# Kernel optimization log

Hardware: AMD Instinct MI355X
Metric: run time of the kernel (lower is better)

The kernel has to match this reference:

```python
import jax, jax.numpy as jnp
import numpy as np

B, IN, H = 8192, 1024, 2048

def setup_inputs() -> dict:
    key = jax.random.key(0)
    k1, k2, k3, k4, k5 = jax.random.split(key, 5)
    prev_state = jax.random.normal(k1, (B, H), dtype=jnp.float32)
    x = jax.random.normal(k2, (B, IN), dtype=jnp.float32)
    input_weights = jax.random.normal(k3, (H, IN), dtype=jnp.float32) / IN ** 0.5
    input_bias = jnp.zeros((H,), dtype=jnp.float32)
    recurrent_weights = jax.random.normal(k4, (H, H), dtype=jnp.float32) / H ** 0.5
    U_z = jax.random.normal(k5, (H, H), dtype=jnp.float32) / H ** 0.5
    b_u = jnp.zeros((H,), dtype=jnp.float32)
    return {"prev_state": prev_state, "input": x,
            "input_weights": input_weights, "input_bias": input_bias,
            "recurrent_weights": recurrent_weights, "U_z": U_z, "b_u": b_u}

def reference(prev_state, input, input_weights, input_bias, recurrent_weights, U_z, b_u):
    # z = tanh(x @ W_x^T + b_x)
    z = jnp.tanh(input @ input_weights.T + input_bias)
    # u = sigmoid(h @ W_h^T + z @ U_z^T + b_u)
    u = jax.nn.sigmoid(prev_state @ recurrent_weights.T + z @ U_z.T + b_u)
    # convex combination of previous state and candidate
    state = u * prev_state + (1.0 - u) * z
    return state
```

## Files before the change

kernel.cpp:

```cpp
#include <hip/hip_runtime.h>
#include <hip/hip_bf16.h>
#include <cstdint>
#include <cstddef>

#define DEVFN static __device__ __forceinline__

typedef __attribute__((ext_vector_type(8))) short bf16x8;
typedef __attribute__((ext_vector_type(4))) float f32x4;

static constexpr int kB = 8192;
static constexpr int kIN = 1024;
static constexpr int kH = 2048;

DEVFN unsigned short f32_to_bf16(float f) {
  union { float f; unsigned int u; } v; v.f = f;
  unsigned int x = v.u;
  x += 0x7fffu + ((x >> 16) & 1u);
  return (unsigned short)(x >> 16);
}
DEVFN float bf16_to_f32(unsigned short u) {
  union { unsigned int u; float f; } v; v.u = (unsigned int)u << 16;
  return v.f;
}

__global__ void cast_strided(const float* __restrict__ src, unsigned short* __restrict__ dst,
                             int n, int srcWshift, int dstStride, int dstOff) {
  int i = (blockIdx.x * blockDim.x + threadIdx.x) * 4;
  if (i >= n) return;
  float4 v = *(const float4*)(src + i);
  int row = i >> srcWshift;
  int col = i - (row << srcWshift);
  unsigned short* d = dst + (size_t)row * dstStride + dstOff + col;
  ushort4 o;
  o.x = f32_to_bf16(v.x); o.y = f32_to_bf16(v.y);
  o.z = f32_to_bf16(v.z); o.w = f32_to_bf16(v.w);
  *(ushort4*)d = o;
}

typedef const __attribute__((address_space(1))) unsigned int* gptr_t;
typedef __attribute__((address_space(3))) unsigned int* lptr_t;
DEVFN void gload16(const unsigned short* g, unsigned short* l) {
  __builtin_amdgcn_global_load_lds((gptr_t)g, (lptr_t)l, 16, 0, 0);
}

DEVFN void barpin() {
  __builtin_amdgcn_s_barrier();
  __builtin_amdgcn_sched_barrier(0);
}
#define LGKM0() asm volatile("s_waitcnt lgkmcnt(0)" ::: "memory")
#define VMC4()  asm volatile("s_waitcnt vmcnt(4)" ::: "memory")


template<int BUF, int QM>
DEVFN void ldA(bf16x8 (&a)[4][2], const unsigned short* lds, int wm, int lr, int lg) {
  const unsigned short* rg = lds + (size_t)(BUF * 4 + wm) * 8192;
#pragma unroll
  for (int mi = 0; mi < 4; ++mi) {
    const int rl = QM * 64 + mi * 16 + lr;
#pragma unroll
    for (int kk = 0; kk < 2; ++kk) {
      const int kel = (kk * 32 + lg * 8) ^ ((rl & 7) * 8);
      a[mi][kk] = *(const bf16x8*)(rg + rl * 64 + kel);
    }
  }
}

template<int BUF, int QN>
DEVFN void ldB(bf16x8 (&b)[4][2], const unsigned short* lds, int wn, int lr, int lg) {
  const unsigned short* rg = lds + (size_t)(BUF * 4 + 2 + (wn >> 1)) * 8192;
#pragma unroll
  for (int ni = 0; ni < 2; ++ni) {
    const int n = QN * 2 + ni;
    const int cl = (wn & 1) * 64 + n * 16 + lr;
#pragma unroll
    for (int kk = 0; kk < 2; ++kk) {
      const int kel = (kk * 32 + lg * 8) ^ ((cl & 7) * 8);
      b[n][kk] = *(const bf16x8*)(rg + cl * 64 + kel);
    }
  }
}

template<int QM, int QN>
DEVFN void mfmaQ(f32x4 (&acc)[8][4], bf16x8 (&a)[4][2], bf16x8 (&b)[4][2]) {
  __builtin_amdgcn_s_setprio(1);
#pragma unroll
  for (int mi = 0; mi < 4; ++mi)
#pragma unroll
    for (int ni = 0; ni < 2; ++ni)
#pragma unroll
      for (int kk = 0; kk < 2; ++kk)
        acc[QM * 4 + mi][QN * 2 + ni] = __builtin_amdgcn_mfma_f32_16x16x32_bf16(
            a[mi][kk], b[QN * 2 + ni][kk], acc[QM * 4 + mi][QN * 2 + ni], 0, 0, 0);
  __builtin_amdgcn_s_setprio(0);
}

template<int EPI>
__global__ __launch_bounds__(512, 2)
void gemm256(const unsigned short* __restrict__ A,
             const unsigned short* __restrict__ W,
             const float* __restrict__ bias,
             int M, int K,
             unsigned short* __restrict__ zBuf, int ldz,
             const float* __restrict__ hIn,
             float* __restrict__ out, int ldo)
{
  __shared__ unsigned short lds[8][8192];
  unsigned short* L = &lds[0][0];

  const int nTM = M >> 8;
  const int bm = blockIdx.x % nTM, bn = blockIdx.x / nTM;
  const int rowBase = bm << 8, colBase = bn << 8;

  const int t = threadIdx.x;
  const int l = t & 63;
  const int w = t >> 6;
  const int lr = l & 15, lg = l >> 4;
  const int wm = w >> 2, wn = w & 3;

  const int srow = t >> 3;
  const int scol = (t & 7) * 8;
  const int kcSrc = scol ^ ((srow & 7) * 8);
  const unsigned short* gA = A + (size_t)(rowBase + srow) * K + kcSrc;
  const unsigned short* gB = W + (size_t)(colBase + srow) * K + kcSrc;

#define STAGE(BUF, OP, HALF, KT) do {                                          \
    const unsigned short* gs = ((OP) ? gB : gA)                                \
        + (size_t)((HALF) * 128) * K + (size_t)(KT) * 64;                      \
    unsigned short* ld = L + (size_t)((BUF) * 4 + (OP) * 2 + (HALF)) * 8192    \
        + w * 512;                                                             \
    gload16(gs, ld);                                                           \
    gload16(gs + (size_t)64 * K, ld + 4096);                                   \
  } while (0)

  f32x4 acc[8][4] = {};
  bf16x8 a[4][2], b[4][2];

  STAGE(0, 0, 0, 0); STAGE(0, 0, 1, 0); STAGE(0, 1, 0, 0); STAGE(0, 1, 1, 0);
  STAGE(1, 1, 0, 1); STAGE(1, 1, 1, 1);
  VMC4();
  barpin();

  const int NP = K >> 7;
  for (int i = 0; i < NP; ++i) {
    const bool more = (i + 1 < NP);
    const int ktb1  = 2 * i + 1;
    const int kt0n  = more ? 2 * i + 2 : 2 * i;
    const int kt1n  = more ? 2 * i + 3 : 2 * i + 1;

    ldA<0, 0>(a, L, wm, lr, lg); ldB<0, 0>(b, L, wn, lr, lg);
    STAGE(1, 0, 0, ktb1);
    barpin(); LGKM0();
    mfmaQ<0, 0>(acc, a, b);
    barpin();
    ldB<0, 1>(b, L, wn, lr, lg);
    STAGE(1, 0, 1, ktb1);
    barpin(); LGKM0();
    mfmaQ<0, 1>(acc, a, b);
    barpin();
    ldA<0, 1>(a, L, wm, lr, lg);
    STAGE(0, 1, 0, kt0n);
    barpin(); LGKM0();
    mfmaQ<1, 0>(acc, a, b);
    barpin();
    STAGE(0, 1, 1, kt0n);
    barpin(); LGKM0();
    mfmaQ<1, 1>(acc, a, b);
    VMC4();
    barpin();
    ldA<1, 0>(a, L, wm, lr, lg); ldB<1, 0>(b, L, wn, lr, lg);
    STAGE(0, 0, 0, kt0n);
    barpin(); LGKM0();
    mfmaQ<0, 0>(acc, a, b);
    barpin();
    ldB<1, 1>(b, L, wn, lr, lg);
    STAGE(0, 0, 1, kt0n);
    barpin(); LGKM0();
    mfmaQ<0, 1>(acc, a, b);
    barpin();
    ldA<1, 1>(a, L, wm, lr, lg);
    STAGE(1, 1, 0, kt1n);
    barpin(); LGKM0();
    mfmaQ<1, 0>(acc, a, b);
    barpin();
    STAGE(1, 1, 1, kt1n);
    barpin(); LGKM0();
    mfmaQ<1, 1>(acc, a, b);
    VMC4();
    barpin();
  }
#undef STAGE

#pragma unroll
  for (int m = 0; m < 8; ++m) {
    const int r0 = rowBase + wm * 128 + m * 16 + lg * 4;
#pragma unroll
    for (int n = 0; n < 4; ++n) {
      const int c = colBase + wn * 64 + n * 16 + lr;
      const float bs = bias[c];
#pragma unroll
      for (int q = 0; q < 4; ++q) {
        const int r = r0 + q;
        const float pre = acc[m][n][q] + bs;
        if (EPI == 0) {
          zBuf[(size_t)r * ldz + c] = f32_to_bf16(tanhf(pre));
        } else {
          const float u = 1.0f / (1.0f + __expf(-pre));
          const float h = hIn[(size_t)r * ldo + c];
          const float z = bf16_to_f32(zBuf[(size_t)r * ldz + c]);
          out[(size_t)r * ldo + c] = u * h + (1.0f - u) * z;
        }
      }
    }
  }
}

extern "C" void kernel_launch(void* const* d_in, const int* in_sizes, int n_in,
                              void* d_out, int out_size, void* d_ws, size_t ws_size,
                              hipStream_t stream) {
  const float* h  = (const float*)d_in[0];
  const float* x  = (const float*)d_in[1];
  const float* Wx = (const float*)d_in[2];
  const float* bx = (const float*)d_in[3];
  const float* Wh = (const float*)d_in[4];
  const float* Uz = (const float*)d_in[5];
  const float* bu = (const float*)d_in[6];
  float* out = (float*)d_out;

  unsigned short* ws   = (unsigned short*)d_ws;
  unsigned short* xb   = ws;
  unsigned short* Wxb  = xb + (size_t)kB * kIN;
  unsigned short* Wcat = Wxb + (size_t)kH * kIN;
  unsigned short* Acat = Wcat + (size_t)kH * 2 * kH;

  const int thr = 256;
  cast_strided<<<(kB * kIN / 4) / thr, thr, 0, stream>>>(x,  xb,   kB * kIN, 10, kIN,    0);
  cast_strided<<<(kH * kIN / 4) / thr, thr, 0, stream>>>(Wx, Wxb,  kH * kIN, 10, kIN,    0);
  cast_strided<<<(kH * kH  / 4) / thr, thr, 0, stream>>>(Wh, Wcat, kH * kH,  11, 2 * kH, 0);
  cast_strided<<<(kH * kH  / 4) / thr, thr, 0, stream>>>(Uz, Wcat, kH * kH,  11, 2 * kH, kH);
  cast_strided<<<(kB * kH  / 4) / thr, thr, 0, stream>>>(h,  Acat, kB * kH,  11, 2 * kH, 0);

  const int grid = (kB / 256) * (kH / 256);

  gemm256<0><<<grid, 512, 0, stream>>>(
      xb, Wxb, bx, kB, kIN, Acat + kH, 2 * kH, nullptr, nullptr, 0);

  gemm256<1><<<grid, 512, 0, stream>>>(
      Acat, Wcat, bu, kB, 2 * kH, Acat + kH, 2 * kH, h, out, kH);
}
```

Baseline: 220.8 us.

## Fuse cast kernels, read h as bf16 in epilogue, relax scheduling pins

Replaces the five separate fp32-to-bf16 cast launches with one kernel that picks source and destination by thread index range. This removes per-launch overhead and tail gaps between launches. The gate epilogue now reads the previous state from the already-cast bf16 buffer instead of the fp32 input, which moves fewer bytes but combines the state at lower precision. It also drops the sched_barrier pins around the workgroup barriers and lowers the occupancy hint in launch_bounds to one block, giving the compiler more registers and scheduling freedom, at the risk of a worse instruction order in the main loop.

```diff
diff --git a/kernel.cpp b/kernel.cpp
--- a/kernel.cpp
+++ b/kernel.cpp
@@ -23,14 +23,22 @@
   return v.f;
 }
 
-__global__ void cast_strided(const float* __restrict__ src, unsigned short* __restrict__ dst,
-                             int n, int srcWshift, int dstStride, int dstOff) {
-  int i = (blockIdx.x * blockDim.x + threadIdx.x) * 4;
-  if (i >= n) return;
-  float4 v = *(const float4*)(src + i);
-  int row = i >> srcWshift;
-  int col = i - (row << srcWshift);
-  unsigned short* d = dst + (size_t)row * dstStride + dstOff + col;
+__global__ void cast_all(const float* __restrict__ x, const float* __restrict__ Wx,
+                         const float* __restrict__ Wh, const float* __restrict__ Uz,
+                         const float* __restrict__ h,
+                         unsigned short* __restrict__ xb, unsigned short* __restrict__ Wxb,
+                         unsigned short* __restrict__ Wcat, unsigned short* __restrict__ Acat) {
+  const long i = (long)blockIdx.x * blockDim.x + threadIdx.x;
+  const float* src; unsigned short* dst; int sh, stride, off; long li;
+  if (i < 2097152L)      { li = i;            src = x;  dst = xb;   sh = 8; stride = 1024; off = 0; }
+  else if (i < 2621440L) { li = i - 2097152L; src = Wx; dst = Wxb;  sh = 8; stride = 1024; off = 0; }
+  else if (i < 3670016L) { li = i - 2621440L; src = Wh; dst = Wcat; sh = 9; stride = 4096; off = 0; }
+  else if (i < 4718592L) { li = i - 3670016L; src = Uz; dst = Wcat; sh = 9; stride = 4096; off = 2048; }
+  else                   { li = i - 4718592L; src = h;  dst = Acat; sh = 9; stride = 4096; off = 0; }
+  float4 v = *(const float4*)(src + li * 4);
+  const long row = li >> sh;
+  const long col = (li & ((1L << sh) - 1)) * 4;
+  unsigned short* d = dst + row * stride + off + col;
   ushort4 o;
   o.x = f32_to_bf16(v.x); o.y = f32_to_bf16(v.y);
   o.z = f32_to_bf16(v.z); o.w = f32_to_bf16(v.w);
@@ -43,10 +51,7 @@
   __builtin_amdgcn_global_load_lds((gptr_t)g, (lptr_t)l, 16, 0, 0);
 }
 
-DEVFN void barpin() {
-  __builtin_amdgcn_s_barrier();
-  __builtin_amdgcn_sched_barrier(0);
-}
+DEVFN void bar() { __builtin_amdgcn_s_barrier(); }
 #define LGKM0() asm volatile("s_waitcnt lgkmcnt(0)" ::: "memory")
 #define VMC4()  asm volatile("s_waitcnt vmcnt(4)" ::: "memory")
 
@@ -95,13 +100,13 @@
 }
 
 template<int EPI>
-__global__ __launch_bounds__(512, 2)
+__global__ __launch_bounds__(512, 1)
 void gemm256(const unsigned short* __restrict__ A,
              const unsigned short* __restrict__ W,
              const float* __restrict__ bias,
              int M, int K,
-             unsigned short* __restrict__ zBuf, int ldz,
-             const float* __restrict__ hIn,
+             unsigned short* __restrict__ zOut,
+             const unsigned short* __restrict__ hzBuf, int ldhz,
              float* __restrict__ out, int ldo)
 {
   __shared__ unsigned short lds[8][8192];
@@ -138,7 +143,7 @@
   STAGE(0, 0, 0, 0); STAGE(0, 0, 1, 0); STAGE(0, 1, 0, 0); STAGE(0, 1, 1, 0);
   STAGE(1, 1, 0, 1); STAGE(1, 1, 1, 1);
   VMC4();
-  barpin();
+  bar();
 
   const int NP = K >> 7;
   for (int i = 0; i < NP; ++i) {
@@ -149,44 +154,44 @@
 
     ldA<0, 0>(a, L, wm, lr, lg); ldB<0, 0>(b, L, wn, lr, lg);
     STAGE(1, 0, 0, ktb1);
-    barpin(); LGKM0();
+    bar(); LGKM0();
     mfmaQ<0, 0>(acc, a, b);
-    barpin();
+    bar();
     ldB<0, 1>(b, L, wn, lr, lg);
     STAGE(1, 0, 1, ktb1);
-    barpin(); LGKM0();
+    bar(); LGKM0();
     mfmaQ<0, 1>(acc, a, b);
-    barpin();
+    bar();
     ldA<0, 1>(a, L, wm, lr, lg);
     STAGE(0, 1, 0, kt0n);
-    barpin(); LGKM0();
+    bar(); LGKM0();
     mfmaQ<1, 0>(acc, a, b);
-    barpin();
+    bar();
     STAGE(0, 1, 1, kt0n);
-    barpin(); LGKM0();
+    bar(); LGKM0();
     mfmaQ<1, 1>(acc, a, b);
     VMC4();
-    barpin();
+    bar();
     ldA<1, 0>(a, L, wm, lr, lg); ldB<1, 0>(b, L, wn, lr, lg);
     STAGE(0, 0, 0, kt0n);
-    barpin(); LGKM0();
+    bar(); LGKM0();
     mfmaQ<0, 0>(acc, a, b);
-    barpin();
+    bar();
     ldB<1, 1>(b, L, wn, lr, lg);
     STAGE(0, 0, 1, kt0n);
-    barpin(); LGKM0();
+    bar(); LGKM0();
     mfmaQ<0, 1>(acc, a, b);
-    barpin();
+    bar();
     ldA<1, 1>(a, L, wm, lr, lg);
     STAGE(1, 1, 0, kt1n);
-    barpin(); LGKM0();
+    bar(); LGKM0();
     mfmaQ<1, 0>(acc, a, b);
-    barpin();
+    bar();
     STAGE(1, 1, 1, kt1n);
-    barpin(); LGKM0();
+    bar(); LGKM0();
     mfmaQ<1, 1>(acc, a, b);
     VMC4();
-    barpin();
+    bar();
   }
 #undef STAGE
 
@@ -202,12 +207,12 @@
         const int r = r0 + q;
         const float pre = acc[m][n][q] + bs;
         if (EPI == 0) {
-          zBuf[(size_t)r * ldz + c] = f32_to_bf16(tanhf(pre));
+          zOut[(size_t)r * ldhz + c] = f32_to_bf16(tanhf(pre));
         } else {
           const float u = 1.0f / (1.0f + __expf(-pre));
-          const float h = hIn[(size_t)r * ldo + c];
-          const float z = bf16_to_f32(zBuf[(size_t)r * ldz + c]);
-          out[(size_t)r * ldo + c] = u * h + (1.0f - u) * z;
+          const float hv = bf16_to_f32(hzBuf[(size_t)r * ldhz + c]);
+          const float zv = bf16_to_f32(hzBuf[(size_t)r * ldhz + 2048 + c]);
+          out[(size_t)r * ldo + c] = u * hv + (1.0f - u) * zv;
         }
       }
     }
@@ -232,18 +237,13 @@
   unsigned short* Wcat = Wxb + (size_t)kH * kIN;
   unsigned short* Acat = Wcat + (size_t)kH * 2 * kH;
 
-  const int thr = 256;
-  cast_strided<<<(kB * kIN / 4) / thr, thr, 0, stream>>>(x,  xb,   kB * kIN, 10, kIN,    0);
-  cast_strided<<<(kH * kIN / 4) / thr, thr, 0, stream>>>(Wx, Wxb,  kH * kIN, 10, kIN,    0);
-  cast_strided<<<(kH * kH  / 4) / thr, thr, 0, stream>>>(Wh, Wcat, kH * kH,  11, 2 * kH, 0);
-  cast_strided<<<(kH * kH  / 4) / thr, thr, 0, stream>>>(Uz, Wcat, kH * kH,  11, 2 * kH, kH);
-  cast_strided<<<(kB * kH  / 4) / thr, thr, 0, stream>>>(h,  Acat, kB * kH,  11, 2 * kH, 0);
+  cast_all<<<34816, 256, 0, stream>>>(x, Wx, Wh, Uz, h, xb, Wxb, Wcat, Acat);
 
   const int grid = (kB / 256) * (kH / 256);
 
   gemm256<0><<<grid, 512, 0, stream>>>(
-      xb, Wxb, bx, kB, kIN, Acat + kH, 2 * kH, nullptr, nullptr, 0);
+      xb, Wxb, bx, kB, kIN, Acat + kH, nullptr, 2 * kH, nullptr, 0);
 
   gemm256<1><<<grid, 512, 0, stream>>>(
-      Acat, Wcat, bu, kB, 2 * kH, Acat + kH, 2 * kH, h, out, kH);
-}
+      Acat, Wcat, bu, kB, 2 * kH, nullptr, Acat, 2 * kH, out, kH);
+}
```

Measured after the change: 211.4 us. 4.3% less time.
